# Kernel tuning notes

Measured on AMD Instinct MI355X. Metric: run time of the kernel, lower is better.

The kernel has to match this reference:

```python
import jax, jax.numpy as jnp
import numpy as np
from jax import lax

B, S, D = 1, 512, 2048
HK, HV, DK, DV, K = 8, 16, 128, 128, 4
R = HV // HK
KEY_DIM = HK * DK
VAL_DIM = HV * DV
CONV_DIM = 2 * KEY_DIM + VAL_DIM
EPS = 1e-6


def setup_inputs() -> dict:
    key = jax.random.key(0)
    ks = jax.random.split(key, 8)
    hidden_states = jax.random.normal(ks[0], (B, S, D), jnp.float32)
    W_qkvz = jax.random.normal(ks[1], (D, 2 * KEY_DIM + 2 * VAL_DIM), jnp.float32) * 0.02
    W_ba = jax.random.normal(ks[2], (D, 2 * HV), jnp.float32) * 0.02
    conv_w = jax.random.normal(ks[3], (CONV_DIM, 1, K), jnp.float32) * 0.2  # depthwise [C,1,K]
    dt_bias = jnp.ones((HV,), jnp.float32)
    A_log = jnp.log(jax.random.uniform(ks[4], (HV,), jnp.float32, 1e-3, 16.0))
    norm_weight = jnp.ones((DV,), jnp.float32)
    W_out = jax.random.normal(ks[5], (VAL_DIM, D), jnp.float32) * 0.02
    return dict(hidden_states=hidden_states, W_qkvz=W_qkvz, W_ba=W_ba, conv_w=conv_w,
                dt_bias=dt_bias, A_log=A_log, norm_weight=norm_weight, W_out=W_out)


def _l2norm(x):
    return x * lax.rsqrt(jnp.sum(x * x, -1, keepdims=True) + EPS)


def reference(hidden_states, W_qkvz, W_ba, conv_w, dt_bias, A_log, norm_weight, W_out):
    # input projections
    qkvz = hidden_states @ W_qkvz              # [B,S,2*key_dim+2*value_dim]
    ba = hidden_states @ W_ba                  # [B,S,2*HV]
    # _rearrange: split per key-head group
    qkvz = qkvz.reshape(B, S, HK, 2 * DK + 2 * R * DV)
    q = qkvz[..., :DK]                                         # [B,S,HK,DK]
    k = qkvz[..., DK:2 * DK]                                   # [B,S,HK,DK]
    v = qkvz[..., 2 * DK:2 * DK + R * DV].reshape(B, S, HV, DV)
    z = qkvz[..., 2 * DK + R * DV:].reshape(B, S, HV, DV)
    ba = ba.reshape(B, S, HK, 2 * R)
    b = ba[..., :R].reshape(B, S, HV)
    a = ba[..., R:].reshape(B, S, HV)
    # fused causal depthwise conv1d + SiLU over concat(q,k,v)
    mixed = jnp.concatenate([q.reshape(B, S, -1), k.reshape(B, S, -1), v.reshape(B, S, -1)], -1)
    mixed = mixed.transpose(0, 2, 1)           # [B,C,S]
    mixed = lax.conv_general_dilated(mixed, conv_w, (1,), [(K - 1, 0)],
                                     feature_group_count=CONV_DIM,
                                     dimension_numbers=('NCH', 'OIH', 'NCH'))
    mixed = jax.nn.silu(mixed).transpose(0, 2, 1)  # [B,S,C]
    q = mixed[..., :KEY_DIM].reshape(B, S, HK, DK)
    k = mixed[..., KEY_DIM:2 * KEY_DIM].reshape(B, S, HK, DK)
    v = mixed[..., 2 * KEY_DIM:].reshape(B, S, HV, DV)
    # gates
    beta = jax.nn.sigmoid(b)                                   # [B,S,HV]
    g = jnp.exp(-jnp.exp(A_log) * jax.nn.softplus(a + dt_bias))  # per-step decay in (0,1)
    q = _l2norm(q) * (DK ** -0.5)
    k = _l2norm(k)
    q = jnp.repeat(q, R, axis=2)               # GQA expand to HV heads
    k = jnp.repeat(k, R, axis=2)
    # gated delta-rule recurrence over sequence (state per batch/head: [DK,DV])
    def step(Sst, inp):
        qt, kt, vt, gt, bt = inp
        Sst = Sst * gt[..., None, None]
        pred = jnp.einsum('bhk,bhkv->bhv', kt, Sst)
        delta = (vt - pred) * bt[..., None]
        Sst = Sst + jnp.einsum('bhk,bhv->bhkv', kt, delta)
        o = jnp.einsum('bhk,bhkv->bhv', qt, Sst)
        return Sst, o
    xs = (q.transpose(1, 0, 2, 3), k.transpose(1, 0, 2, 3), v.transpose(1, 0, 2, 3),
          g.transpose(1, 0, 2), beta.transpose(1, 0, 2))
    S0 = jnp.zeros((B, HV, DK, DV), jnp.float32)
    _, core = lax.scan(step, S0, xs)           # core: [S,B,HV,DV]
    core = core.transpose(1, 0, 2, 3)          # [B,S,HV,DV]
    # gated RMSNorm per value head, gated by silu(z)
    var = jnp.mean(core * core, -1, keepdims=True)
    normed = core * lax.rsqrt(var + EPS) * norm_weight * jax.nn.silu(z)
    return normed.reshape(B, S, VAL_DIM) @ W_out
```

## Files before the change

kernel.cpp:

```cpp
#include <hip/hip_runtime.h>
#include <hip/hip_bf16.h>
#include <math.h>

#define S_  512
#define D_  2048
#define HK_ 8
#define HV_ 16
#define DK_ 128
#define DV_ 128
#define KEY_DIM_ 1024
#define VAL_DIM_ 2048
#define QKVZ_N  6144
#define EPS_ 1e-6f
#define SPAD_ (S_ + 8)

typedef __attribute__((ext_vector_type(8))) short short8;
typedef __attribute__((ext_vector_type(4))) float f32x4;
typedef unsigned short ushort_t;
typedef unsigned int uint_t;

__device__ __forceinline__ ushort_t f2bf(float x) {
    uint_t u = __float_as_uint(x);
    return (ushort_t)((u + 0x7FFFu + ((u >> 16) & 1u)) >> 16);
}

__device__ __forceinline__ void gl2lds16(const void* g, void* l) {
    __builtin_amdgcn_global_load_lds((const __attribute__((address_space(1))) uint_t*)g,
                                     (__attribute__((address_space(3))) uint_t*)l, 16, 0, 0);
}
__device__ __forceinline__ void gl2lds4(const void* g, void* l) {
    __builtin_amdgcn_global_load_lds((const __attribute__((address_space(1))) uint_t*)g,
                                     (__attribute__((address_space(3))) uint_t*)l, 4, 0, 0);
}

#define RL(x, l) __int_as_float(__builtin_amdgcn_readlane(__float_as_int(x), (l)))

__device__ __forceinline__ void transpose_body(const float* __restrict__ W,
                                               ushort_t* __restrict__ Th,
                                               int K, int N, int kb, int nb,
                                               int t, float* smem) {
    float (*tile)[65] = (float(*)[65])smem;
#pragma unroll
    for (int i = 0; i < 4; ++i) {
        int r = (t >> 4) + i * 16;
        int c4 = (t & 15) * 4;
        float4 v = *(const float4*)&W[(size_t)(kb + r) * N + nb + c4];
        tile[r][c4 + 0] = v.x; tile[r][c4 + 1] = v.y;
        tile[r][c4 + 2] = v.z; tile[r][c4 + 3] = v.w;
    }
    __syncthreads();
#pragma unroll
    for (int i = 0; i < 2; ++i) {
        int idx = t + 256 * i;
        int n = idx >> 3;
        int k8 = (idx & 7) * 8;
        ushort_t p[8];
#pragma unroll
        for (int r = 0; r < 8; ++r) p[r] = f2bf(tile[k8 + r][n]);
        *(uint4*)&Th[(size_t)(nb + n) * K + kb + k8] = *(const uint4*)p;
    }
}

__global__ __launch_bounds__(256) void prep_kernel(const float* __restrict__ hidden,
                                                   const float* __restrict__ W_qkvz,
                                                   const float* __restrict__ W_out,
                                                   const float* __restrict__ Wba,
                                                   ushort_t* __restrict__ hidh,
                                                   ushort_t* __restrict__ Wqh,
                                                   ushort_t* __restrict__ Woh,
                                                   float* __restrict__ ba) {
    __shared__ float smem[64 * 65];
    const int id = blockIdx.x;
    const int t = threadIdx.x;

    if (id < 1024) {
        int i = id * 256 + t;
        float4 v = ((const float4*)hidden)[i];
        ushort4 h;
        h.x = f2bf(v.x); h.y = f2bf(v.y); h.z = f2bf(v.z); h.w = f2bf(v.w);
        ((ushort4*)hidh)[i] = h;
    } else if (id < 1024 + 3072) {
        int lid = id - 1024;
        transpose_body(W_qkvz, Wqh, D_, QKVZ_N, (lid / 96) * 64, (lid % 96) * 64, t, smem);
    } else if (id < 1024 + 3072 + 1024) {
        int lid = id - 4096;
        transpose_body(W_out, Woh, D_, D_, (lid / 32) * 64, (lid % 32) * 64, t, smem);
    } else {
        const int s = id - 5120;
        const int j = t & 31;
        const int kg = t >> 5;
        const float* h = hidden + (size_t)s * D_;
        float sum = 0.f;
        const int k0 = kg * 256;
#pragma unroll 8
        for (int k = k0; k < k0 + 256; ++k)
            sum = fmaf(h[k], Wba[(size_t)k * 32 + j], sum);
        float (*red)[32] = (float(*)[32])smem;
        red[kg][j] = sum;
        __syncthreads();
        if (t < 32) {
            float tot = 0.f;
#pragma unroll
            for (int r = 0; r < 8; ++r) tot += red[r][j];
            ba[s * 32 + j] = tot;
        }
    }
}

template<int BM, int BN, int WR, int WC>
__global__ __launch_bounds__(256) void gemm_bf16(const ushort_t* __restrict__ A,
                                                 const ushort_t* __restrict__ B,
                                                 float* __restrict__ C,
                                                 int M, int N, int K) {
    constexpr int TM = BM / (16 * WR);
    constexpr int TN = BN / (16 * WC);
    constexpr int AI = (BM / 16) * 2;
    constexpr int BI = (BN / 16) * 2;

    __shared__ __align__(16) ushort_t sA[2][2][BM][32];
    __shared__ __align__(16) ushort_t sB[2][2][BN][32];

    const int t = threadIdx.x;
    const int w = t >> 6, lane = t & 63;
    const int wr = w / WC, wc = w % WC;
    const int lm = lane & 15, quad = lane >> 4;
    const int m0 = blockIdx.y * BM, n0 = blockIdx.x * BN;
    const int lrow = lane >> 2;
    const int lch  = (lane & 3) * 8;

    auto stage = [&](int buf, int k0) {
#pragma unroll
        for (int j = w; j < AI; j += 4) {
            int ks = j & 1, r0 = (j >> 1) * 16;
            gl2lds16(&A[(size_t)(m0 + r0 + lrow) * K + k0 + ks * 32 + lch],
                     &sA[buf][ks][r0][0]);
        }
#pragma unroll
        for (int j = w; j < BI; j += 4) {
            int ks = j & 1, r0 = (j >> 1) * 16;
            gl2lds16(&B[(size_t)(n0 + r0 + lrow) * K + k0 + ks * 32 + lch],
                     &sB[buf][ks][r0][0]);
        }
    };

    f32x4 acc[TM][TN] = {};
    stage(0, 0);
    __syncthreads();

    const int NK = K / 64;
    for (int it = 0; it < NK; ++it) {
        int buf = it & 1;
        if (it + 1 < NK) stage(buf ^ 1, (it + 1) * 64);
#pragma unroll
        for (int ks = 0; ks < 2; ++ks) {
            short8 bf[TN];
#pragma unroll
            for (int ni = 0; ni < TN; ++ni)
                bf[ni] = *(const short8*)&sB[buf][ks][wc * (TN * 16) + ni * 16 + lm][quad * 8];
#pragma unroll
            for (int mi = 0; mi < TM; ++mi) {
                short8 af = *(const short8*)&sA[buf][ks][wr * (TM * 16) + mi * 16 + lm][quad * 8];
#pragma unroll
                for (int ni = 0; ni < TN; ++ni)
                    acc[mi][ni] = __builtin_amdgcn_mfma_f32_16x16x32_bf16(af, bf[ni], acc[mi][ni], 0, 0, 0);
            }
        }
        __syncthreads();
    }

#pragma unroll
    for (int mi = 0; mi < TM; ++mi)
#pragma unroll
        for (int ni = 0; ni < TN; ++ni) {
            int row = m0 + wr * TM * 16 + mi * 16 + quad * 4;
            int col = n0 + wc * TN * 16 + ni * 16 + lm;
#pragma unroll
            for (int r = 0; r < 4; ++r)
                C[(size_t)(row + r) * N + col] = acc[mi][ni][r];
        }
}

__global__ __launch_bounds__(128) void conv_kernel(const float* __restrict__ qkvz,
                                                   const float* __restrict__ conv_w,
                                                   float* __restrict__ qc,
                                                   float* __restrict__ kc,
                                                   float* __restrict__ vc) {
    const int s   = blockIdx.x;
    const int grp = blockIdx.y;
    const int d   = threadIdx.x;

    int col, c;
    if (grp < 8) {
        int hk = grp;
        col = hk * 768 + d;
        c   = hk * 128 + d;
    } else if (grp < 16) {
        int hk = grp - 8;
        col = hk * 768 + 128 + d;
        c   = 1024 + (hk * 128 + d);
    } else {
        int hv = grp - 16;
        col = (hv >> 1) * 768 + 256 + (hv & 1) * 128 + d;
        c   = 2048 + (hv * 128 + d);
    }

    const float w0 = conv_w[c * 4 + 0];
    const float w1 = conv_w[c * 4 + 1];
    const float w2 = conv_w[c * 4 + 2];
    const float w3 = conv_w[c * 4 + 3];

    float x = 0.f;
    if (s - 3 >= 0) x += qkvz[(size_t)(s - 3) * QKVZ_N + col] * w0;
    if (s - 2 >= 0) x += qkvz[(size_t)(s - 2) * QKVZ_N + col] * w1;
    if (s - 1 >= 0) x += qkvz[(size_t)(s - 1) * QKVZ_N + col] * w2;
    x += qkvz[(size_t)s * QKVZ_N + col] * w3;

    x = x / (1.f + expf(-x));

    if (grp < 16) {
        float ss = x * x;
#pragma unroll
        for (int m = 1; m < 64; m <<= 1) ss += __shfl_xor(ss, m);
        __shared__ float red[2];
        int wid = threadIdx.x >> 6;
        if ((threadIdx.x & 63) == 0) red[wid] = ss;
        __syncthreads();
        float tot = red[0] + red[1];
        float scale = rsqrtf(tot + EPS_);
        if (grp < 8) {
            x = x * scale * 0.08838834764831845f;
            qc[((size_t)s * HK_ + grp) * DK_ + d] = x;
        } else {
            x = x * scale;
            kc[((size_t)s * HK_ + (grp - 8)) * DK_ + d] = x;
        }
    } else {
        vc[((size_t)s * HV_ + (grp - 16)) * DV_ + d] = x;
    }
}

template<int CTRL>
__device__ __forceinline__ float dpp_xor(float x) {
    int v = __builtin_amdgcn_update_dpp(0, __float_as_int(x), CTRL, 0xF, 0xF, true);
    return __int_as_float(v);
}
__device__ __forceinline__ float red16(float x) {
    x += dpp_xor<0xB1>(x);
    x += dpp_xor<0x4E>(x);
    x += dpp_xor<0x141>(x);
    x += dpp_xor<0x140>(x);
    return x;
}
__device__ __forceinline__ float red32(float x) {
    x = red16(x);
    x += __int_as_float(__builtin_amdgcn_ds_swizzle(__float_as_int(x), 0x401F));
    return x;
}

__device__ __forceinline__ float gate_g(float a, float Aexp) {
    float sp = (a > 20.f) ? a : log1pf(expf(a));
    return expf(-Aexp * sp);
}

__global__ __launch_bounds__(256) void scal_kernel(const float* __restrict__ kc,
                                                   const float* __restrict__ qc,
                                                   const float* __restrict__ ba,
                                                   const float* __restrict__ A_log,
                                                   const float* __restrict__ dt_bias,
                                                   float* __restrict__ scal) {
    const int t  = blockIdx.x;
    const int hk = threadIdx.x >> 5;
    const int l  = threadIdx.x & 31;

    const float* kt = &kc[((size_t)t * HK_ + hk) * DK_ + l * 4];
    const float* qt = &qc[((size_t)t * HK_ + hk) * DK_ + l * 4];
    const float4 zz = {0.f, 0.f, 0.f, 0.f};
    float4 k0 = *(const float4*)kt;
    float4 q0 = *(const float4*)qt;
    float4 k1 = (t >= 1) ? *(const float4*)(kt - (size_t)HK_ * DK_)     : zz;
    float4 k2 = (t >= 2) ? *(const float4*)(kt - (size_t)2 * HK_ * DK_) : zz;
    float4 k3 = (t >= 3) ? *(const float4*)(kt - (size_t)3 * HK_ * DK_) : zz;

    auto dot4 = [](float4 a, float4 b) { return a.x*b.x + a.y*b.y + a.z*b.z + a.w*b.w; };
    float c1 = red32(dot4(k0, k1));
    float c2 = red32(dot4(k0, k2));
    float c3 = red32(dot4(k0, k3));
    float d0 = red32(dot4(q0, k0));
    float d1 = red32(dot4(q0, k1));
    float d2 = red32(dot4(q0, k2));
    float d3 = red32(dot4(q0, k3));

    if (l < 2) {
        int h = hk * 2 + l;
        float Aexp = expf(A_log[h]);
        float dtb  = dt_bias[h];
        float bv = ba[t * 32 + hk * 4 + l];
        float av = ba[t * 32 + hk * 4 + 2 + l];
        float be = 1.f / (1.f + expf(-bv));
        float g0 = gate_g(av + dtb, Aexp);
        float g1 = 1.f, g2 = 1.f, g3 = 1.f;
        if (t >= 1) g1 = gate_g(ba[(t - 1) * 32 + hk * 4 + 2 + l] + dtb, Aexp);
        if (t >= 2) g2 = gate_g(ba[(t - 2) * 32 + hk * 4 + 2 + l] + dtb, Aexp);
        if (t >= 3) g3 = gate_g(ba[(t - 3) * 32 + hk * 4 + 2 + l] + dtb, Aexp);
        float G2 = g0 * g1, G3 = G2 * g2, G4 = G3 * g3;
        float4 oC = {g0, be, G4, 0.f};
        float4 oA = {-be * g0 * c1, -be * G2 * c2, -be * G3 * c3, -be * G4};
        float4 oB = {d0, g0 * d1, G2 * d2, G3 * d3};
        float* dst = &scal[(size_t)(h * SPAD_ + t) * 16];
        *(float4*)&dst[0]  = oC;
        *(float4*)&dst[4]  = oA;
        *(float4*)&dst[8]  = oB;
        *(float4*)&dst[12] = zz;
    }
}

__global__ __launch_bounds__(128) void scan_kernel(const float* __restrict__ qc,
                                                   const float* __restrict__ kc,
                                                   const float* __restrict__ vc,
                                                   const float* __restrict__ scal,
                                                   float* __restrict__ core) {
    const int h = blockIdx.y, v0 = blockIdx.x * 8;
    const int tid = threadIdx.x;
    const int w = tid >> 6, lane = tid & 63;
    const int sub = lane & 15, colg = lane >> 4;
    const int vloc = w * 4 + colg;
    const int v = v0 + vloc;
    const int hk = h >> 1;

    __shared__ __align__(16) float skq[2][32][256];
    __shared__ __align__(16) float sv[2][32][8];
    __shared__ __align__(16) float hkq[2][4][256];
    __shared__ __align__(16) float hvb[2][4][8];

    auto stage_chunk = [&](int buf, int c) {
        const int t0 = c * 32;
        for (int j = w * 16; j < w * 16 + 16; ++j) {
            int tt = t0 + j;
            const float* src = (lane < 32)
                ? &kc[((size_t)tt * HK_ + hk) * DK_ + lane * 4]
                : &qc[((size_t)tt * HK_ + hk) * DK_ + (lane - 32) * 4];
            gl2lds16(src, &skq[buf][j][0]);
        }
        if (w == 0) {
#pragma unroll
            for (int i = 0; i < 4; ++i) {
                int tt = t0 + i * 8 + (lane >> 3);
                gl2lds4(&vc[((size_t)tt * HV_ + h) * DV_ + v0 + (lane & 7)],
                        &sv[buf][i * 8][0]);
            }
        }
    };
    auto stage_head = [&](int c) {
        const int hb = c & 1;
        const int t0 = c * 32;
        if (w == 1) {
#pragma unroll
            for (int j = 0; j < 4; ++j) {
                int tt = t0 + j;
                const float* src = (lane < 32)
                    ? &kc[((size_t)tt * HK_ + hk) * DK_ + lane * 4]
                    : &qc[((size_t)tt * HK_ + hk) * DK_ + (lane - 32) * 4];
                gl2lds16(src, &hkq[hb][j][0]);
            }
        } else {
            if (lane < 32)
                gl2lds4(&vc[((size_t)(t0 + (lane >> 3)) * HV_ + h) * DV_ + v0 + (lane & 7)],
                        &hvb[hb][0][0]);
        }
    };

    auto ldsc = [&](int c, float4& o0, float4& o1, float4& o2) {
        const float* p = &scal[(size_t)(h * SPAD_ + c * 32 + (lane & 31)) * 16];
        o0 = *(const float4*)p;
        o1 = *(const float4*)(p + 4);
        o2 = *(const float4*)(p + 8);
    };

    f32x4 Sr[2] = {};
    f32x4 kR[8][2] = {}, qR[4][2] = {};
    float vR[4] = {}, U[4] = {}, V[4] = {}, dl[4] = {};
    float4 cur0 = {0,0,0,0}, cur1 = {0,0,0,0}, cur2 = {0,0,0,0};
    float4 nxt0 = {0,0,0,0}, nxt1 = {0,0,0,0}, nxt2 = {0,0,0,0};
    float4 prv0 = {0,0,0,0};

    stage_chunk(0, 0);
    stage_head(1);
    ldsc(0, cur0, cur1, cur2);
    ldsc(1, nxt0, nxt1, nxt2);
    __syncthreads();

#pragma unroll
    for (int p = 0; p < 4; ++p) {
        kR[p][0] = *(const f32x4*)&skq[0][p][4 * sub];
        kR[p][1] = *(const f32x4*)&skq[0][p][64 + 4 * sub];
        qR[p][0] = *(const f32x4*)&skq[0][p][128 + 4 * sub];
        qR[p][1] = *(const f32x4*)&skq[0][p][192 + 4 * sub];
    }
    vR[0] = sv[0][0][vloc];
    vR[1] = sv[0][1][vloc];

    for (int c = 0; c < 16; ++c) {
        const int buf = c & 1;
        const int hb = (c + 1) & 1;
        if (c + 1 < 16) stage_chunk(buf ^ 1, c + 1);
        if (c + 2 < 16) stage_head(c + 2);
        const int t0 = c * 32;

#pragma unroll
        for (int j = 0; j < 32; ++j) {
            {
                const float g  = (j >= 2) ? RL(cur0.x, j - 2) : RL(prv0.x, 30 + j);
                const float dd = dl[(j + 2) & 3];
                const f32x4 g4 = {g, g, g, g};
                const f32x4 dd4 = {dd, dd, dd, dd};
                Sr[0] = kR[(j + 6) & 7][0] * dd4 + g4 * Sr[0];
                Sr[1] = kR[(j + 6) & 7][1] * dd4 + g4 * Sr[1];
            }
            {
                const float* kb = (j < 28) ? &skq[buf][j + 4][0] : &hkq[hb][j - 28][0];
                kR[(j + 4) & 7][0] = *(const f32x4*)&kb[4 * sub];
                kR[(j + 4) & 7][1] = *(const f32x4*)&kb[64 + 4 * sub];
                qR[(j + 4) & 3][0] = *(const f32x4*)&kb[128 + 4 * sub];
                qR[(j + 4) & 3][1] = *(const f32x4*)&kb[192 + 4 * sub];
            }
            vR[(j + 2) & 3] = (j < 30) ? sv[buf][j + 2][vloc] : hvb[hb][j - 30][vloc];
            {
                f32x4 ku = kR[(j + 2) & 7][0] * Sr[0] + kR[(j + 2) & 7][1] * Sr[1];
                f32x4 qu = qR[(j + 2) & 3][0] * Sr[0] + qR[(j + 2) & 3][1] * Sr[1];
                U[(j + 2) & 3] = red16((ku[0] + ku[1]) + (ku[2] + ku[3]));
                V[(j + 2) & 3] = red16((qu[0] + qu[1]) + (qu[2] + qu[3]));
            }
            {
                const float be = RL(cur0.y, j), G4 = RL(cur0.z, j);
                const float a1 = RL(cur1.x, j), a2 = RL(cur1.y, j);
                const float a3 = RL(cur1.z, j), bU = RL(cur1.w, j);
                const float w0 = RL(cur2.x, j), w1 = RL(cur2.y, j);
                const float w2 = RL(cur2.z, j), w3 = RL(cur2.w, j);
                const float d1 = dl[(j + 3) & 3], d2 = dl[(j + 2) & 3], d3 = dl[(j + 1) & 3];
                const float E = fmaf(bU, U[j & 3], be * vR[j & 3]);
                const float X = fmaf(a2, d2, fmaf(a3, d3, E));
                const float dn = fmaf(a1, d1, X);
                const float o = fmaf(w0, dn, fmaf(w1, d1,
                                  fmaf(w2, d2, fmaf(w3, d3, G4 * V[j & 3]))));
                if (sub == 0)
                    core[((size_t)(t0 + j) * HV_ + h) * DV_ + v] = o;
                dl[j & 3] = dn;
            }
        }
        __syncthreads();
        prv0 = cur0;
        cur0 = nxt0; cur1 = nxt1; cur2 = nxt2;
        if (c + 2 < 16) ldsc(c + 2, nxt0, nxt1, nxt2);
    }
}

__global__ __launch_bounds__(128) void normgate_kernel(const float* __restrict__ core,
                                                       const float* __restrict__ qkvz,
                                                       const float* __restrict__ nw,
                                                       ushort_t* __restrict__ nh) {
    const int s  = blockIdx.x;
    const int hv = blockIdx.y;
    const int d  = threadIdx.x;

    float x = core[((size_t)s * HV_ + hv) * DV_ + d];
    float ss = x * x;
#pragma unroll
    for (int m = 1; m < 64; m <<= 1) ss += __shfl_xor(ss, m);
    __shared__ float red[2];
    int wid = threadIdx.x >> 6;
    if ((threadIdx.x & 63) == 0) red[wid] = ss;
    __syncthreads();
    float var = (red[0] + red[1]) * (1.f / 128.f);
    float rs  = rsqrtf(var + EPS_);

    float z  = qkvz[(size_t)s * QKVZ_N + (hv >> 1) * 768 + 512 + (hv & 1) * 128 + d];
    float sz = z / (1.f + expf(-z));

    float y = x * rs * nw[d] * sz;
    nh[(size_t)s * VAL_DIM_ + hv * DV_ + d] = f2bf(y);
}

extern "C" void kernel_launch(void* const* d_in, const int* in_sizes, int n_in,
                              void* d_out, int out_size, void* d_ws, size_t ws_size,
                              hipStream_t stream) {
    const float* hidden  = (const float*)d_in[0];
    const float* W_qkvz  = (const float*)d_in[1];
    const float* W_ba    = (const float*)d_in[2];
    const float* conv_w  = (const float*)d_in[3];
    const float* dt_bias = (const float*)d_in[4];
    const float* A_log   = (const float*)d_in[5];
    const float* norm_w  = (const float*)d_in[6];
    const float* W_out   = (const float*)d_in[7];
    float* out = (float*)d_out;

    char* w = (char*)d_ws;
    auto alloc = [&](size_t bytes) { char* p = w; w += (bytes + 255) & ~(size_t)255; return p; };

    float*    qkvz = (float*)alloc((size_t)S_ * QKVZ_N * 4);
    float*    ba   = (float*)alloc((size_t)S_ * 32 * 4);
    float*    qc   = (float*)alloc((size_t)SPAD_ * KEY_DIM_ * 4);
    float*    kc   = (float*)alloc((size_t)SPAD_ * KEY_DIM_ * 4);
    float*    vc   = (float*)alloc((size_t)SPAD_ * VAL_DIM_ * 4);
    float*    scal = (float*)alloc((size_t)HV_ * SPAD_ * 16 * 4);
    float*    core = (float*)alloc((size_t)S_ * VAL_DIM_ * 4);
    ushort_t* hidh = (ushort_t*)alloc((size_t)S_ * D_ * 2);
    ushort_t* nrmh = (ushort_t*)alloc((size_t)S_ * VAL_DIM_ * 2);
    ushort_t* Wqh  = (ushort_t*)alloc((size_t)D_ * QKVZ_N * 2);
    ushort_t* Woh  = (ushort_t*)alloc((size_t)VAL_DIM_ * D_ * 2);

    prep_kernel<<<dim3(5632), 256, 0, stream>>>(hidden, W_qkvz, W_out, W_ba,
                                                hidh, Wqh, Woh, ba);

    gemm_bf16<64, 128, 1, 4><<<dim3(QKVZ_N / 128, S_ / 64), 256, 0, stream>>>(
        hidh, Wqh, qkvz, S_, QKVZ_N, D_);

    conv_kernel<<<dim3(S_, 32), 128, 0, stream>>>(qkvz, conv_w, qc, kc, vc);

    scal_kernel<<<dim3(S_), 256, 0, stream>>>(kc, qc, ba, A_log, dt_bias, scal);

    scan_kernel<<<dim3(DV_ / 8, HV_), 128, 0, stream>>>(qc, kc, vc, scal, core);

    normgate_kernel<<<dim3(S_, HV_), 128, 0, stream>>>(core, qkvz, norm_w, nrmh);

    gemm_bf16<64, 64, 2, 2><<<dim3(D_ / 64, S_ / 64), 256, 0, stream>>>(
        nrmh, Woh, out, S_, D_, VAL_DIM_);
}
```

Before: 296.7 us.

## Replace LDS staging in scan with direct global register prefetch, single-wave blocks

The scan kernel drops its shared-memory double-buffered staging of k/q/v and the per-chunk barrier. Each lane now prefetches k, q and v straight from global memory into a rotating register ring six steps ahead. Blocks shrink to one wave covering 4 value columns, which doubles the grid. This removes __syncthreads and LDS traffic from the serial recurrence, but exposes it to global/L2 load latency and adds redundant loads across blocks.

```diff
diff --git a/kernel.cpp b/kernel.cpp
--- a/kernel.cpp
+++ b/kernel.cpp
@@ -314,100 +314,53 @@
     }
 }
 
-__global__ __launch_bounds__(128) void scan_kernel(const float* __restrict__ qc,
-                                                   const float* __restrict__ kc,
-                                                   const float* __restrict__ vc,
-                                                   const float* __restrict__ scal,
-                                                   float* __restrict__ core) {
-    const int h = blockIdx.y, v0 = blockIdx.x * 8;
-    const int tid = threadIdx.x;
-    const int w = tid >> 6, lane = tid & 63;
+__global__ __launch_bounds__(64) void scan_kernel(const float* __restrict__ qc,
+                                                  const float* __restrict__ kc,
+                                                  const float* __restrict__ vc,
+                                                  const float* __restrict__ scal,
+                                                  float* __restrict__ core) {
+    const int h = blockIdx.y, v0 = blockIdx.x * 4;
+    const int lane = threadIdx.x;
     const int sub = lane & 15, colg = lane >> 4;
-    const int vloc = w * 4 + colg;
-    const int v = v0 + vloc;
+    const int v = v0 + colg;
     const int hk = h >> 1;
 
-    __shared__ __align__(16) float skq[2][32][256];
-    __shared__ __align__(16) float sv[2][32][8];
-    __shared__ __align__(16) float hkq[2][4][256];
-    __shared__ __align__(16) float hvb[2][4][8];
-
-    auto stage_chunk = [&](int buf, int c) {
-        const int t0 = c * 32;
-        for (int j = w * 16; j < w * 16 + 16; ++j) {
-            int tt = t0 + j;
-            const float* src = (lane < 32)
-                ? &kc[((size_t)tt * HK_ + hk) * DK_ + lane * 4]
-                : &qc[((size_t)tt * HK_ + hk) * DK_ + (lane - 32) * 4];
-            gl2lds16(src, &skq[buf][j][0]);
-        }
-        if (w == 0) {
-#pragma unroll
-            for (int i = 0; i < 4; ++i) {
-                int tt = t0 + i * 8 + (lane >> 3);
-                gl2lds4(&vc[((size_t)tt * HV_ + h) * DV_ + v0 + (lane & 7)],
-                        &sv[buf][i * 8][0]);
-            }
-        }
-    };
-    auto stage_head = [&](int c) {
-        const int hb = c & 1;
-        const int t0 = c * 32;
-        if (w == 1) {
-#pragma unroll
-            for (int j = 0; j < 4; ++j) {
-                int tt = t0 + j;
-                const float* src = (lane < 32)
-                    ? &kc[((size_t)tt * HK_ + hk) * DK_ + lane * 4]
-                    : &qc[((size_t)tt * HK_ + hk) * DK_ + (lane - 32) * 4];
-                gl2lds16(src, &hkq[hb][j][0]);
-            }
-        } else {
-            if (lane < 32)
-                gl2lds4(&vc[((size_t)(t0 + (lane >> 3)) * HV_ + h) * DV_ + v0 + (lane & 7)],
-                        &hvb[hb][0][0]);
-        }
-    };
-
-    auto ldsc = [&](int c, float4& o0, float4& o1, float4& o2) {
-        const float* p = &scal[(size_t)(h * SPAD_ + c * 32 + (lane & 31)) * 16];
-        o0 = *(const float4*)p;
-        o1 = *(const float4*)(p + 4);
-        o2 = *(const float4*)(p + 8);
-    };
-
     f32x4 Sr[2] = {};
-    f32x4 kR[8][2] = {}, qR[4][2] = {};
-    float vR[4] = {}, U[4] = {}, V[4] = {}, dl[4] = {};
+    f32x4 kR[8][2] = {}, qR[8][2] = {};
+    float vR[8] = {};
+    float U[4] = {}, V[4] = {}, dl[4] = {};
     float4 cur0 = {0,0,0,0}, cur1 = {0,0,0,0}, cur2 = {0,0,0,0};
     float4 nxt0 = {0,0,0,0}, nxt1 = {0,0,0,0}, nxt2 = {0,0,0,0};
     float4 prv0 = {0,0,0,0};
 
-    stage_chunk(0, 0);
-    stage_head(1);
-    ldsc(0, cur0, cur1, cur2);
-    ldsc(1, nxt0, nxt1, nxt2);
-    __syncthreads();
-
-#pragma unroll
-    for (int p = 0; p < 4; ++p) {
-        kR[p][0] = *(const f32x4*)&skq[0][p][4 * sub];
-        kR[p][1] = *(const f32x4*)&skq[0][p][64 + 4 * sub];
-        qR[p][0] = *(const f32x4*)&skq[0][p][128 + 4 * sub];
-        qR[p][1] = *(const f32x4*)&skq[0][p][192 + 4 * sub];
-    }
-    vR[0] = sv[0][0][vloc];
-    vR[1] = sv[0][1][vloc];
+#pragma unroll
+    for (int p = 0; p < 6; ++p) {
+        const size_t bo = ((size_t)p * HK_ + hk) * DK_;
+        kR[p][0] = *(const f32x4*)&kc[bo + 4 * sub];
+        kR[p][1] = *(const f32x4*)&kc[bo + 64 + 4 * sub];
+        qR[p][0] = *(const f32x4*)&qc[bo + 4 * sub];
+        qR[p][1] = *(const f32x4*)&qc[bo + 64 + 4 * sub];
+        vR[p] = vc[((size_t)p * HV_ + h) * DV_ + v];
+    }
+    {
+        const float* p = &scal[(size_t)(h * SPAD_ + (lane & 31)) * 16];
+        cur0 = *(const float4*)p;
+        cur1 = *(const float4*)(p + 4);
+        cur2 = *(const float4*)(p + 8);
+    }
 
     for (int c = 0; c < 16; ++c) {
-        const int buf = c & 1;
-        const int hb = (c + 1) & 1;
-        if (c + 1 < 16) stage_chunk(buf ^ 1, c + 1);
-        if (c + 2 < 16) stage_head(c + 2);
+        if (c + 1 < 16) {
+            const float* p = &scal[(size_t)(h * SPAD_ + (c + 1) * 32 + (lane & 31)) * 16];
+            nxt0 = *(const float4*)p;
+            nxt1 = *(const float4*)(p + 4);
+            nxt2 = *(const float4*)(p + 8);
+        }
         const int t0 = c * 32;
 
 #pragma unroll
         for (int j = 0; j < 32; ++j) {
+            const int t = t0 + j;
             {
                 const float g  = (j >= 2) ? RL(cur0.x, j - 2) : RL(prv0.x, 30 + j);
                 const float dd = dl[(j + 2) & 3];
@@ -417,16 +370,16 @@
                 Sr[1] = kR[(j + 6) & 7][1] * dd4 + g4 * Sr[1];
             }
             {
-                const float* kb = (j < 28) ? &skq[buf][j + 4][0] : &hkq[hb][j - 28][0];
-                kR[(j + 4) & 7][0] = *(const f32x4*)&kb[4 * sub];
-                kR[(j + 4) & 7][1] = *(const f32x4*)&kb[64 + 4 * sub];
-                qR[(j + 4) & 3][0] = *(const f32x4*)&kb[128 + 4 * sub];
-                qR[(j + 4) & 3][1] = *(const f32x4*)&kb[192 + 4 * sub];
+                const size_t bo = ((size_t)(t + 6) * HK_ + hk) * DK_;
+                kR[(j + 6) & 7][0] = *(const f32x4*)&kc[bo + 4 * sub];
+                kR[(j + 6) & 7][1] = *(const f32x4*)&kc[bo + 64 + 4 * sub];
+                qR[(j + 6) & 7][0] = *(const f32x4*)&qc[bo + 4 * sub];
+                qR[(j + 6) & 7][1] = *(const f32x4*)&qc[bo + 64 + 4 * sub];
+                vR[(j + 6) & 7] = vc[((size_t)(t + 6) * HV_ + h) * DV_ + v];
             }
-            vR[(j + 2) & 3] = (j < 30) ? sv[buf][j + 2][vloc] : hvb[hb][j - 30][vloc];
             {
                 f32x4 ku = kR[(j + 2) & 7][0] * Sr[0] + kR[(j + 2) & 7][1] * Sr[1];
-                f32x4 qu = qR[(j + 2) & 3][0] * Sr[0] + qR[(j + 2) & 3][1] * Sr[1];
+                f32x4 qu = qR[(j + 2) & 7][0] * Sr[0] + qR[(j + 2) & 7][1] * Sr[1];
                 U[(j + 2) & 3] = red16((ku[0] + ku[1]) + (ku[2] + ku[3]));
                 V[(j + 2) & 3] = red16((qu[0] + qu[1]) + (qu[2] + qu[3]));
             }
@@ -437,20 +390,18 @@
                 const float w0 = RL(cur2.x, j), w1 = RL(cur2.y, j);
                 const float w2 = RL(cur2.z, j), w3 = RL(cur2.w, j);
                 const float d1 = dl[(j + 3) & 3], d2 = dl[(j + 2) & 3], d3 = dl[(j + 1) & 3];
-                const float E = fmaf(bU, U[j & 3], be * vR[j & 3]);
+                const float E = fmaf(bU, U[j & 3], be * vR[j & 7]);
                 const float X = fmaf(a2, d2, fmaf(a3, d3, E));
                 const float dn = fmaf(a1, d1, X);
                 const float o = fmaf(w0, dn, fmaf(w1, d1,
                                   fmaf(w2, d2, fmaf(w3, d3, G4 * V[j & 3]))));
                 if (sub == 0)
-                    core[((size_t)(t0 + j) * HV_ + h) * DV_ + v] = o;
+                    core[((size_t)t * HV_ + h) * DV_ + v] = o;
                 dl[j & 3] = dn;
             }
         }
-        __syncthreads();
         prv0 = cur0;
         cur0 = nxt0; cur1 = nxt1; cur2 = nxt2;
-        if (c + 2 < 16) ldsc(c + 2, nxt0, nxt1, nxt2);
     }
 }
 
@@ -518,7 +469,7 @@
 
     scal_kernel<<<dim3(S_), 256, 0, stream>>>(kc, qc, ba, A_log, dt_bias, scal);
 
-    scan_kernel<<<dim3(DV_ / 8, HV_), 128, 0, stream>>>(qc, kc, vc, scal, core);
+    scan_kernel<<<dim3(DV_ / 4, HV_), 64, 0, stream>>>(qc, kc, vc, scal, core);
 
     normgate_kernel<<<dim3(S_, HV_), 128, 0, stream>>>(core, qkvz, norm_w, nrmh);
 
```

Measured after the change: 300.2 us. About the same (+1.2%).
